# Kernel tuning notes

Hardware: AMD Instinct MI355X
Metric: run time of the kernel (lower is better)

## Reference

```python
import jax, jax.numpy as jnp
import numpy as np

B, L, D, H, FF, NS = 4, 1024, 1024, 16, 4096, 64
HD = D // H
EPS = 1e-5


def layer_norm(x, g, b):
    mu = jnp.mean(x, axis=-1, keepdims=True)
    var = jnp.mean(jnp.square(x - mu), axis=-1, keepdims=True)
    return (x - mu) * jax.lax.rsqrt(var + EPS) * g + b


def mha(xq, xkv, wqkv, bqkv, wo, bo, bias=None):
    # torch nn.MultiheadAttention with packed in_proj: rows [0:D]=Q, [D:2D]=K, [2D:3D]=V
    Bq, Lq, Dm = xq.shape
    q = (xq @ wqkv[:Dm].T + bqkv[:Dm]).reshape(Bq, Lq, H, HD).transpose(0, 2, 1, 3)
    k = (xkv @ wqkv[Dm:2 * Dm].T + bqkv[Dm:2 * Dm]).reshape(Bq, -1, H, HD).transpose(0, 2, 1, 3)
    v = (xkv @ wqkv[2 * Dm:].T + bqkv[2 * Dm:]).reshape(Bq, -1, H, HD).transpose(0, 2, 1, 3)
    scores = jnp.einsum('bhqd,bhkd->bhqk', q, k) / np.sqrt(HD).astype(np.float32)
    if bias is not None:
        scores = scores + bias.reshape(Bq, H, Lq, -1)
    attn = jax.nn.softmax(scores, axis=-1)
    out = jnp.einsum('bhqk,bhkd->bhqd', attn, v).transpose(0, 2, 1, 3).reshape(Bq, Lq, Dm)
    return out @ wo.T + bo


def setup_inputs() -> dict:
    key = jax.random.key(0)
    ks = jax.random.split(key, 16)
    w = lambda k, shape: jax.random.normal(k, shape, jnp.float32) * 0.02
    return {
        'x': jax.random.normal(ks[0], (B, L, D), jnp.float32),
        'alibi_bias': jax.random.normal(ks[1], (B * H, L, L), jnp.float32) * 0.1,
        'species_emb': jax.random.normal(ks[2], (B, NS, D), jnp.float32),
        'norm1_g': jnp.ones(D), 'norm1_b': jnp.zeros(D),
        'sa_wqkv': w(ks[3], (3 * D, D)), 'sa_bqkv': jnp.zeros(3 * D),
        'sa_wo': w(ks[4], (D, D)), 'sa_bo': jnp.zeros(D),
        'ca_nq_g': jnp.ones(D), 'ca_nq_b': jnp.zeros(D),
        'ca_nkv_g': jnp.ones(D), 'ca_nkv_b': jnp.zeros(D),
        'ca_wqkv': w(ks[5], (3 * D, D)), 'ca_bqkv': jnp.zeros(3 * D),
        'ca_wo': w(ks[6], (D, D)), 'ca_bo': jnp.zeros(D),
        'gate_param': jnp.float32(0.1),
        'ffn_g': jnp.ones(D), 'ffn_b': jnp.zeros(D),
        'ffn_w1': w(ks[7], (2 * FF, D)), 'ffn_b1': jnp.zeros(2 * FF),
        'ffn_w2': w(ks[8], (D, FF)), 'ffn_b2': jnp.zeros(D),
    }


def reference(x, alibi_bias, species_emb,
              norm1_g, norm1_b, sa_wqkv, sa_bqkv, sa_wo, sa_bo,
              ca_nq_g, ca_nq_b, ca_nkv_g, ca_nkv_b, ca_wqkv, ca_bqkv, ca_wo, ca_bo,
              gate_param, ffn_g, ffn_b, ffn_w1, ffn_b1, ffn_w2, ffn_b2):
    # 1) pre-norm self-attention with ALiBi additive bias
    h = layer_norm(x, norm1_g, norm1_b)
    h = mha(h, h, sa_wqkv, sa_bqkv, sa_wo, sa_bo, bias=alibi_bias)
    x = x + h  # dropout is identity in eval mode
    # 2) gated cross-attention with species embeddings
    q = layer_norm(x, ca_nq_g, ca_nq_b)
    kv = layer_norm(species_emb, ca_nkv_g, ca_nkv_b)
    cross = mha(q, kv, ca_wqkv, ca_bqkv, ca_wo, ca_bo)
    x = x + jax.nn.sigmoid(gate_param) * cross
    # 3) GEGLU feed-forward
    f = layer_norm(x, ffn_g, ffn_b) @ ffn_w1.T + ffn_b1
    val, gate = f[..., :FF], f[..., FF:]
    f = (val * jax.nn.gelu(gate, approximate=False)) @ ffn_w2.T + ffn_b2
    return x + f
```

## Files before the change

### kernel.cpp

```cpp
#include <hip/hip_runtime.h>
#include <hip/hip_bf16.h>
#include <cstdint>

#define DEVI __device__ __forceinline__

typedef __attribute__((ext_vector_type(8))) short  short8;
typedef __attribute__((ext_vector_type(8))) __bf16 bf16x8;
typedef __attribute__((ext_vector_type(4))) float  f32x4;

DEVI float bf2f(short s) {
    unsigned u = ((unsigned)(unsigned short)s) << 16;
    return __builtin_bit_cast(float, u);
}
DEVI short f2bf(float f) {
    unsigned u = __builtin_bit_cast(unsigned, f);
    u = u + 0x7FFF + ((u >> 16) & 1);
    return (short)(u >> 16);
}

#define GLDS(gp, lp) __builtin_amdgcn_global_load_lds( \
    (const __attribute__((address_space(1))) void*)(gp), \
    (__attribute__((address_space(3))) void*)(lp), 16, 0, 0)

__global__ __launch_bounds__(256) void cvt_bf16(const float* src, short* dst, long n) {
    const long i = ((long)blockIdx.x * 256 + threadIdx.x) * 8;
    const float4 a = *(const float4*)&src[i];
    const float4 b = *(const float4*)&src[i + 4];
    short8 o;
    o[0] = f2bf(a.x); o[1] = f2bf(a.y); o[2] = f2bf(a.z); o[3] = f2bf(a.w);
    o[4] = f2bf(b.x); o[5] = f2bf(b.y); o[6] = f2bf(b.z); o[7] = f2bf(b.w);
    *(short8*)&dst[i] = o;
}

struct CvtArgs {
    const float* src[6]; short* dst[6]; int blkStart[7];
};
__global__ __launch_bounds__(256) void cvt_all(CvtArgs c) {
    const int b = blockIdx.x;
    int s = 0;
    while (b >= c.blkStart[s + 1]) s++;
    const long i = ((long)(b - c.blkStart[s]) * 256 + threadIdx.x) * 8;
    const float4 a0 = *(const float4*)&c.src[s][i];
    const float4 a1 = *(const float4*)&c.src[s][i + 4];
    short8 o;
    o[0] = f2bf(a0.x); o[1] = f2bf(a0.y); o[2] = f2bf(a0.z); o[3] = f2bf(a0.w);
    o[4] = f2bf(a1.x); o[5] = f2bf(a1.y); o[6] = f2bf(a1.z); o[7] = f2bf(a1.w);
    *(short8*)&c.dst[s][i] = o;
}

struct GArgs {
    const short* A; long lda, sAb, sAh;
    const short* B; long ldb, sBb, sBh;
    short* C;       long ldc, sCb, sCh;
    const float* bias;
    const float* addm; long ldad, sDb, sDh;
    float* resid;
    float* outf;
    const float* gate;
    const float* addf;
    float scale;
    int K, nh;
};

template<int BM, int BN, int EPI>
__global__ __launch_bounds__(256) void gemm_bt(GArgs a) {
    constexpr int WM = BM / 2, WN = BN / 2, MI = WM / 16, NI = WN / 16;
    __shared__ __align__(16) short As[2][BM * 32];
    __shared__ __align__(16) short Bs[2][BN * 32];
    const int tid = threadIdx.x;
    const int wave = tid >> 6, lane = tid & 63;
    const int wm = (wave >> 1) * WM, wn = (wave & 1) * WN;
    const int q = lane >> 4, r = lane & 15;
    const int gx = gridDim.x, gy = gridDim.y;
    int flat = (int)(blockIdx.y * gx + blockIdx.x);
    { const int cp = (gx * gy) >> 3; flat = (flat & 7) * cp + (flat >> 3); }
    const int bx = flat % gx, by = flat / gx;
    const long bb = blockIdx.z / a.nh, hh = blockIdx.z % a.nh;
    const short* Ab = a.A + bb * a.sAb + hh * a.sAh + (long)by * BM * a.lda;
    const short* Bb = a.B + bb * a.sBb + hh * a.sBh + (long)bx * BN * a.ldb;
    const int trow = tid >> 2;
    const int tcol = (tid & 3) * 8;
    f32x4 acc[MI][NI] = {};
    const int nt = a.K >> 5;

    auto stage = [&](int buf, int k0) {
#pragma unroll
        for (int i = 0; i < BM / 64; i++)
            GLDS(Ab + (long)(i * 64 + trow) * a.lda + k0 + tcol,
                 &As[buf][(i * 64 + trow) * 32 + tcol]);
#pragma unroll
        for (int i = 0; i < BN / 64; i++)
            GLDS(Bb + (long)(i * 64 + trow) * a.ldb + k0 + tcol,
                 &Bs[buf][(i * 64 + trow) * 32 + tcol]);
    };

    stage(0, 0);
    asm volatile("s_waitcnt vmcnt(0)" ::: "memory");
    __builtin_amdgcn_s_barrier();

    int cur = 0;
    for (int t = 0; t < nt; ++t) {
        if (t + 1 < nt) stage(cur ^ 1, (t + 1) << 5);
        bf16x8 av[MI], bv[NI];
#pragma unroll
        for (int mi = 0; mi < MI; mi++)
            av[mi] = __builtin_bit_cast(bf16x8, *(const short8*)&As[cur][(wm + mi * 16 + r) * 32 + q * 8]);
#pragma unroll
        for (int ni = 0; ni < NI; ni++)
            bv[ni] = __builtin_bit_cast(bf16x8, *(const short8*)&Bs[cur][(wn + ni * 16 + r) * 32 + q * 8]);
#pragma unroll
        for (int mi = 0; mi < MI; mi++)
#pragma unroll
            for (int ni = 0; ni < NI; ni++)
                acc[mi][ni] = __builtin_amdgcn_mfma_f32_16x16x32_bf16(av[mi], bv[ni], acc[mi][ni], 0, 0, 0);
        asm volatile("s_waitcnt vmcnt(0) lgkmcnt(0)" ::: "memory");
        __builtin_amdgcn_s_barrier();
        cur ^= 1;
    }

    const long m0 = (long)by * BM + wm;
    const long n0 = (long)bx * BN + wn;
    if constexpr (EPI == 0) {
        short* scrbase = &As[0][0];
        short* scr = scrbase + wave * 16 * (WN + 2);
        short* Cbase = a.C + bb * a.sCb + hh * a.sCh;
        constexpr int LPR = WN / 8;
        constexpr int RPI = 64 / LPR;
        const int srow = lane / LPR, scol = (lane % LPR) * 8;
#pragma unroll
        for (int mi = 0; mi < MI; mi++) {
            asm volatile("s_waitcnt lgkmcnt(0)" ::: "memory");
#pragma unroll
            for (int ni = 0; ni < NI; ni++)
#pragma unroll
                for (int j = 0; j < 4; j++) {
                    float v = acc[mi][ni][j];
                    if (a.bias) v += a.bias[n0 + ni * 16 + r];
                    scr[(q * 4 + j) * (WN + 2) + ni * 16 + r] = f2bf(v);
                }
            asm volatile("s_waitcnt lgkmcnt(0)" ::: "memory");
#pragma unroll
            for (int it = 0; it < 16 / RPI; it++) {
                const int row = it * RPI + srow;
                const short8 vv = *(const short8*)&scr[row * (WN + 2) + scol];
                *(short8*)&Cbase[(m0 + mi * 16 + row) * a.ldc + n0 + scol] = vv;
            }
        }
        return;
    }
    float gs = a.scale;
    if (EPI == 2 && a.gate) gs *= 1.f / (1.f + __expf(-(*a.gate)));
#pragma unroll
    for (int mi = 0; mi < MI; mi++)
#pragma unroll
        for (int ni = 0; ni < NI; ni++)
#pragma unroll
            for (int j = 0; j < 4; j++) {
                const long m = m0 + mi * 16 + q * 4 + j;
                const long n = n0 + ni * 16 + r;
                float v = acc[mi][ni][j];
                if constexpr (EPI == 1) {
                    v *= a.scale;
                    if (a.addm) v += a.addm[bb * a.sDb + hh * a.sDh + m * a.ldad + n];
                    a.C[bb * a.sCb + hh * a.sCh + m * a.ldc + n] = f2bf(v);
                } else if constexpr (EPI == 2) {
                    if (a.bias) v += a.bias[n];
                    const long idx = m * a.ldc + n;
                    const float base = a.addf ? a.addf[idx] : a.resid[idx];
                    a.resid[idx] = base + gs * v;
                } else if constexpr (EPI == 3) {
                    if (a.bias) v += a.bias[n];
                    a.outf[m * a.ldc + n] = a.resid[m * a.ldc + n] + v;
                }
            }
}

struct GGArgs {
    const short* A; long lda;
    const short* Bv; const short* Bg; long ldb;
    short* C; long ldc;
    const float* b1;
    int K;
};
__global__ __launch_bounds__(256) void gemm_geglu(GGArgs a) {
    constexpr int BM = 128, BN = 64, WM = 64, WN = 32, MI = 4, NI = 2;
    __shared__ __align__(16) short As[2][BM * 32];
    __shared__ __align__(16) short Bs[2][BN * 32];
    __shared__ __align__(16) short Gs[2][BN * 32];
    const int tid = threadIdx.x;
    const int wave = tid >> 6, lane = tid & 63;
    const int wm = (wave >> 1) * WM, wn = (wave & 1) * WN;
    const int q = lane >> 4, r = lane & 15;
    const int gx = gridDim.x, gy = gridDim.y;
    int flat = (int)(blockIdx.y * gx + blockIdx.x);
    { const int cp = (gx * gy) >> 3; flat = (flat & 7) * cp + (flat >> 3); }
    const int bx = flat % gx, by = flat / gx;
    const short* Ab = a.A + (long)by * BM * a.lda;
    const short* Bb = a.Bv + (long)bx * BN * a.ldb;
    const short* Gb = a.Bg + (long)bx * BN * a.ldb;
    const int trow = tid >> 2, tcol = (tid & 3) * 8;
    f32x4 accv[MI][NI] = {}, accg[MI][NI] = {};
    const int nt = a.K >> 5;

    auto stage = [&](int buf, int k0) {
#pragma unroll
        for (int i = 0; i < 2; i++)
            GLDS(Ab + (long)(i * 64 + trow) * a.lda + k0 + tcol,
                 &As[buf][(i * 64 + trow) * 32 + tcol]);
        GLDS(Bb + (long)trow * a.ldb + k0 + tcol, &Bs[buf][trow * 32 + tcol]);
        GLDS(Gb + (long)trow * a.ldb + k0 + tcol, &Gs[buf][trow * 32 + tcol]);
    };

    stage(0, 0);
    asm volatile("s_waitcnt vmcnt(0)" ::: "memory");
    __builtin_amdgcn_s_barrier();

    int cur = 0;
    for (int t = 0; t < nt; ++t) {
        if (t + 1 < nt) stage(cur ^ 1, (t + 1) << 5);
        bf16x8 av[MI], bv[NI], gv[NI];
#pragma unroll
        for (int mi = 0; mi < MI; mi++)
            av[mi] = __builtin_bit_cast(bf16x8, *(const short8*)&As[cur][(wm + mi * 16 + r) * 32 + q * 8]);
#pragma unroll
        for (int ni = 0; ni < NI; ni++) {
            bv[ni] = __builtin_bit_cast(bf16x8, *(const short8*)&Bs[cur][(wn + ni * 16 + r) * 32 + q * 8]);
            gv[ni] = __builtin_bit_cast(bf16x8, *(const short8*)&Gs[cur][(wn + ni * 16 + r) * 32 + q * 8]);
        }
#pragma unroll
        for (int mi = 0; mi < MI; mi++)
#pragma unroll
            for (int ni = 0; ni < NI; ni++) {
                accv[mi][ni] = __builtin_amdgcn_mfma_f32_16x16x32_bf16(av[mi], bv[ni], accv[mi][ni], 0, 0, 0);
                accg[mi][ni] = __builtin_amdgcn_mfma_f32_16x16x32_bf16(av[mi], gv[ni], accg[mi][ni], 0, 0, 0);
            }
        asm volatile("s_waitcnt vmcnt(0) lgkmcnt(0)" ::: "memory");
        __builtin_amdgcn_s_barrier();
        cur ^= 1;
    }

    const long m0 = (long)by * BM + wm;
    const long n0 = (long)bx * BN + wn;
    short* scr = &As[0][0] + wave * 16 * (WN + 2);
    const int srow = lane >> 2, scol = (lane & 3) * 8;
#pragma unroll
    for (int mi = 0; mi < MI; mi++) {
        asm volatile("s_waitcnt lgkmcnt(0)" ::: "memory");
#pragma unroll
        for (int ni = 0; ni < NI; ni++)
#pragma unroll
            for (int j = 0; j < 4; j++) {
                const long n = n0 + ni * 16 + r;
                const float v = accv[mi][ni][j] + a.b1[n];
                const float g = accg[mi][ni][j] + a.b1[4096 + n];
                const float ge = 0.5f * g * (1.f + erff(g * 0.7071067811865476f));
                scr[(q * 4 + j) * (WN + 2) + ni * 16 + r] = f2bf(v * ge);
            }
        asm volatile("s_waitcnt lgkmcnt(0)" ::: "memory");
        const short8 vv = *(const short8*)&scr[srow * (WN + 2) + scol];
        *(short8*)&a.C[(m0 + mi * 16 + srow) * a.ldc + n0 + scol] = vv;
    }
}

__global__ __launch_bounds__(256) void flash_sa(const short* qkv, const short* vt,
                                                const float* alibi, short* Obuf) {
    __shared__ __align__(16) short Ps[64 * 64];
    __shared__ __align__(16) short Ks[2][64 * 64], Vs[2][64 * 64];
    const int tid = threadIdx.x;
    const int wave = tid >> 6, lane = tid & 63, q = lane >> 4, r = lane & 15;
    int flat = (int)(blockIdx.y * 16 + blockIdx.x);
    flat = (flat & 7) * 128 + (flat >> 3);
    const int qt = flat & 15, bh = flat >> 4, b = bh >> 4, h = bh & 15;
    const long qrow0 = (long)b * 1024 + qt * 64;
    const int rw = tid >> 3, sp = tid & 7;

    auto stage_kv = [&](int buf, int kt) {
#pragma unroll
        for (int i = 0; i < 2; i++) {
            const int row = i * 32 + rw;
            const int c8 = (sp ^ (row & 7)) * 8;
            GLDS(qkv + ((long)b * 1024 + kt * 64 + row) * 3072 + 1024 + h * 64 + c8,
                 &Ks[buf][row * 64 + sp * 8]);
            GLDS(vt + ((long)bh * 64 + row) * 1024 + kt * 64 + c8,
                 &Vs[buf][row * 64 + sp * 8]);
        }
    };

#pragma unroll
    for (int i = 0; i < 2; i++) {
        const int row = i * 32 + rw;
        const int c8 = (sp ^ (row & 7)) * 8;
        GLDS(qkv + (qrow0 + row) * 3072 + h * 64 + c8, &Ps[row * 64 + sp * 8]);
    }
    stage_kv(0, 0);
    asm volatile("s_waitcnt vmcnt(0)" ::: "memory");
    __builtin_amdgcn_s_barrier();

    const int arow = wave * 16 + r;
    bf16x8 qv[2];
#pragma unroll
    for (int kk = 0; kk < 2; kk++)
        qv[kk] = __builtin_bit_cast(bf16x8,
            *(const short8*)&Ps[arow * 64 + (((kk * 4 + q) ^ (arow & 7)) * 8)]);

    f32x4 o[4] = {};
    float m_run[4], l_run[4];
#pragma unroll
    for (int j = 0; j < 4; j++) { m_run[j] = -1e30f; l_run[j] = 0.f; }

    int cur = 0;
    for (int kt = 0; kt < 16; kt++) {
        float al[4][4];
        const float* ab = alibi + (long)bh * 1048576 + (long)(qt * 64 + wave * 16) * 1024 + kt * 64;
#pragma unroll
        for (int ni = 0; ni < 4; ni++)
#pragma unroll
            for (int j = 0; j < 4; j++)
                al[ni][j] = ab[(q * 4 + j) * 1024 + ni * 16 + r];
        if (kt < 15) stage_kv(cur ^ 1, kt + 1);

        f32x4 sacc[4] = {};
        __builtin_amdgcn_s_setprio(1);
#pragma unroll
        for (int kk = 0; kk < 2; kk++) {
#pragma unroll
            for (int ni = 0; ni < 4; ni++) {
                const int brow = ni * 16 + r;
                const bf16x8 bv = __builtin_bit_cast(bf16x8,
                    *(const short8*)&Ks[cur][brow * 64 + (((kk * 4 + q) ^ (brow & 7)) * 8)]);
                sacc[ni] = __builtin_amdgcn_mfma_f32_16x16x32_bf16(qv[kk], bv, sacc[ni], 0, 0, 0);
            }
        }
        __builtin_amdgcn_s_setprio(0);
        float s[4][4];
#pragma unroll
        for (int ni = 0; ni < 4; ni++)
#pragma unroll
            for (int j = 0; j < 4; j++)
                s[ni][j] = sacc[ni][j] * 0.125f + al[ni][j];

        float p[4][4];
#pragma unroll
        for (int j = 0; j < 4; j++) {
            float mx = fmaxf(fmaxf(s[0][j], s[1][j]), fmaxf(s[2][j], s[3][j]));
#pragma unroll
            for (int off = 8; off; off >>= 1) mx = fmaxf(mx, __shfl_xor(mx, off));
            const float newm = fmaxf(m_run[j], mx);
            const float sc = __expf(m_run[j] - newm);
            m_run[j] = newm;
            float rs = 0.f;
#pragma unroll
            for (int ni = 0; ni < 4; ni++) { p[ni][j] = __expf(s[ni][j] - newm); rs += p[ni][j]; }
#pragma unroll
            for (int off = 8; off; off >>= 1) rs += __shfl_xor(rs, off);
            l_run[j] = l_run[j] * sc + rs;
#pragma unroll
            for (int nd = 0; nd < 4; nd++) o[nd][j] *= sc;
        }

#pragma unroll
        for (int ni = 0; ni < 4; ni++)
#pragma unroll
            for (int j = 0; j < 4; j++) {
                const int row = wave * 16 + q * 4 + j;
                const int col = ni * 16 + r;
                const int scol = (((col >> 3) ^ (row & 7)) << 3) | (col & 7);
                Ps[row * 64 + scol] = f2bf(p[ni][j]);
            }
        asm volatile("s_waitcnt lgkmcnt(0)" ::: "memory");

        const int prow = wave * 16 + r;
        __builtin_amdgcn_s_setprio(1);
#pragma unroll
        for (int kk = 0; kk < 2; kk++) {
            const bf16x8 pa = __builtin_bit_cast(bf16x8,
                *(const short8*)&Ps[prow * 64 + (((kk * 4 + q) ^ (prow & 7)) * 8)]);
#pragma unroll
            for (int nd = 0; nd < 4; nd++) {
                const int vrow = nd * 16 + r;
                const bf16x8 vv = __builtin_bit_cast(bf16x8,
                    *(const short8*)&Vs[cur][vrow * 64 + (((kk * 4 + q) ^ (vrow & 7)) * 8)]);
                o[nd] = __builtin_amdgcn_mfma_f32_16x16x32_bf16(pa, vv, o[nd], 0, 0, 0);
            }
        }
        __builtin_amdgcn_s_setprio(0);
        asm volatile("s_waitcnt vmcnt(0) lgkmcnt(0)" ::: "memory");
        __builtin_amdgcn_s_barrier();
        cur ^= 1;
    }

    short* scr = &Ps[wave * 1024];
#pragma unroll
    for (int j = 0; j < 4; j++) {
        const float li = 1.f / l_run[j];
#pragma unroll
        for (int nd = 0; nd < 4; nd++)
            scr[(q * 4 + j) * 64 + nd * 16 + r] = f2bf(o[nd][j] * li);
    }
    asm volatile("s_waitcnt lgkmcnt(0)" ::: "memory");
    const int srow = lane >> 3, scol = (lane & 7) * 8;
#pragma unroll
    for (int it = 0; it < 2; it++) {
        const int row = it * 8 + srow;
        const short8 vv = *(const short8*)&scr[row * 64 + scol];
        *(short8*)&Obuf[(qrow0 + wave * 16 + row) * 1024 + h * 64 + scol] = vv;
    }
}

__global__ __launch_bounds__(256) void flash_ca(const short* q2, const short* kv2,
                                                const short* vt, short* Obuf) {
    __shared__ __align__(16) short Qs[64 * 64], Ks[64 * 64], Vs[64 * 64], Ps[64 * 64];
    const int tid = threadIdx.x;
    const int wave = tid >> 6, lane = tid & 63, q = lane >> 4, r = lane & 15;
    int flat = (int)(blockIdx.y * 16 + blockIdx.x);
    flat = (flat & 7) * 128 + (flat >> 3);
    const int qt = flat & 15, bh = flat >> 4, b = bh >> 4, h = bh & 15;
    const long qrow0 = (long)b * 1024 + qt * 64;
    const int rw = tid >> 3, sp = tid & 7;

#pragma unroll
    for (int i = 0; i < 2; i++) {
        const int row = i * 32 + rw;
        const int c8 = (sp ^ (row & 7)) * 8;
        GLDS(q2 + (qrow0 + row) * 1024 + h * 64 + c8, &Qs[row * 64 + sp * 8]);
        GLDS(kv2 + ((long)b * 64 + row) * 2048 + h * 64 + c8, &Ks[row * 64 + sp * 8]);
        GLDS(vt + ((long)bh * 64 + row) * 64 + c8, &Vs[row * 64 + sp * 8]);
    }
    asm volatile("s_waitcnt vmcnt(0)" ::: "memory");
    __syncthreads();

    f32x4 sacc[4] = {};
    const int arow = wave * 16 + r;
    __builtin_amdgcn_s_setprio(1);
#pragma unroll
    for (int kk = 0; kk < 2; kk++) {
        const bf16x8 av = __builtin_bit_cast(bf16x8,
            *(const short8*)&Qs[arow * 64 + (((kk * 4 + q) ^ (arow & 7)) * 8)]);
#pragma unroll
        for (int ni = 0; ni < 4; ni++) {
            const int brow = ni * 16 + r;
            const bf16x8 bv = __builtin_bit_cast(bf16x8,
                *(const short8*)&Ks[brow * 64 + (((kk * 4 + q) ^ (brow & 7)) * 8)]);
            sacc[ni] = __builtin_amdgcn_mfma_f32_16x16x32_bf16(av, bv, sacc[ni], 0, 0, 0);
        }
    }
    __builtin_amdgcn_s_setprio(0);
    float p[4][4], linv[4];
#pragma unroll
    for (int j = 0; j < 4; j++) {
        float s0 = sacc[0][j] * 0.125f, s1 = sacc[1][j] * 0.125f;
        float s2 = sacc[2][j] * 0.125f, s3 = sacc[3][j] * 0.125f;
        float mx = fmaxf(fmaxf(s0, s1), fmaxf(s2, s3));
#pragma unroll
        for (int off = 8; off; off >>= 1) mx = fmaxf(mx, __shfl_xor(mx, off));
        p[0][j] = __expf(s0 - mx); p[1][j] = __expf(s1 - mx);
        p[2][j] = __expf(s2 - mx); p[3][j] = __expf(s3 - mx);
        float rs = p[0][j] + p[1][j] + p[2][j] + p[3][j];
#pragma unroll
        for (int off = 8; off; off >>= 1) rs += __shfl_xor(rs, off);
        linv[j] = 1.f / rs;
    }
#pragma unroll
    for (int ni = 0; ni < 4; ni++)
#pragma unroll
        for (int j = 0; j < 4; j++) {
            const int row = wave * 16 + q * 4 + j;
            const int col = ni * 16 + r;
            const int scol = (((col >> 3) ^ (row & 7)) << 3) | (col & 7);
            Ps[row * 64 + scol] = f2bf(p[ni][j]);
        }
    asm volatile("s_waitcnt lgkmcnt(0)" ::: "memory");

    f32x4 o[4] = {};
    const int prow = wave * 16 + r;
    __builtin_amdgcn_s_setprio(1);
#pragma unroll
    for (int kk = 0; kk < 2; kk++) {
        const bf16x8 pa = __builtin_bit_cast(bf16x8,
            *(const short8*)&Ps[prow * 64 + (((kk * 4 + q) ^ (prow & 7)) * 8)]);
#pragma unroll
        for (int nd = 0; nd < 4; nd++) {
            const int vrow = nd * 16 + r;
            const bf16x8 vv = __builtin_bit_cast(bf16x8,
                *(const short8*)&Vs[vrow * 64 + (((kk * 4 + q) ^ (vrow & 7)) * 8)]);
            o[nd] = __builtin_amdgcn_mfma_f32_16x16x32_bf16(pa, vv, o[nd], 0, 0, 0);
        }
    }
    __builtin_amdgcn_s_setprio(0);

    short* scr = &Ps[wave * 1024];
#pragma unroll
    for (int j = 0; j < 4; j++)
#pragma unroll
        for (int nd = 0; nd < 4; nd++)
            scr[(q * 4 + j) * 64 + nd * 16 + r] = f2bf(o[nd][j] * linv[j]);
    asm volatile("s_waitcnt lgkmcnt(0)" ::: "memory");
    const int srow = lane >> 3, scol = (lane & 7) * 8;
#pragma unroll
    for (int it = 0; it < 2; it++) {
        const int row = it * 8 + srow;
        const short8 vv = *(const short8*)&scr[row * 64 + scol];
        *(short8*)&Obuf[(qrow0 + wave * 16 + row) * 1024 + h * 64 + scol] = vv;
    }
}

__global__ __launch_bounds__(256) void ln_rows(const float* X, const float* gw,
                                               const float* bw, short* Y) {
    const long row = blockIdx.x;
    const float* x = X + row * 1024;
    const int t = threadIdx.x;
    float v[4], s1 = 0.f, s2 = 0.f;
#pragma unroll
    for (int i = 0; i < 4; i++) {
        v[i] = x[t + i * 256];
        s1 += v[i]; s2 += v[i] * v[i];
    }
#pragma unroll
    for (int o = 32; o; o >>= 1) { s1 += __shfl_xor(s1, o); s2 += __shfl_xor(s2, o); }
    __shared__ float sm[8];
    if ((t & 63) == 0) { sm[t >> 6] = s1; sm[4 + (t >> 6)] = s2; }
    __syncthreads();
    s1 = sm[0] + sm[1] + sm[2] + sm[3];
    s2 = sm[4] + sm[5] + sm[6] + sm[7];
    const float mu = s1 * (1.f / 1024.f);
    const float var = s2 * (1.f / 1024.f) - mu * mu;
    const float rr = rsqrtf(var + 1e-5f);
#pragma unroll
    for (int i = 0; i < 4; i++) {
        const int c = t + i * 256;
        Y[row * 1024 + c] = f2bf((v[i] - mu) * rr * gw[c] + bw[c]);
    }
}

__global__ __launch_bounds__(256) void softmax1024(short* S) {
    const long row = blockIdx.x;
    short* p = S + row * 1024;
    const int t = threadIdx.x;
    float v[4];
#pragma unroll
    for (int i = 0; i < 4; i++) v[i] = bf2f(p[t + i * 256]);
    float m = fmaxf(fmaxf(v[0], v[1]), fmaxf(v[2], v[3]));
#pragma unroll
    for (int o = 32; o; o >>= 1) m = fmaxf(m, __shfl_xor(m, o));
    __shared__ float sm[4];
    if ((t & 63) == 0) sm[t >> 6] = m;
    __syncthreads();
    m = fmaxf(fmaxf(sm[0], sm[1]), fmaxf(sm[2], sm[3]));
    float e[4], s = 0.f;
#pragma unroll
    for (int i = 0; i < 4; i++) { e[i] = __expf(v[i] - m); s += e[i]; }
#pragma unroll
    for (int o = 32; o; o >>= 1) s += __shfl_xor(s, o);
    __syncthreads();
    if ((t & 63) == 0) sm[t >> 6] = s;
    __syncthreads();
    s = sm[0] + sm[1] + sm[2] + sm[3];
    const float inv = 1.f / s;
#pragma unroll
    for (int i = 0; i < 4; i++) p[t + i * 256] = f2bf(e[i] * inv);
}

__global__ __launch_bounds__(256) void softmax64(short* S) {
    const long row = (long)blockIdx.x * 4 + (threadIdx.x >> 6);
    const int lane = threadIdx.x & 63;
    short* p = S + row * 64;
    float v = bf2f(p[lane]);
    float m = v;
#pragma unroll
    for (int o = 32; o; o >>= 1) m = fmaxf(m, __shfl_xor(m, o));
    float e = __expf(v - m), s = e;
#pragma unroll
    for (int o = 32; o; o >>= 1) s += __shfl_xor(s, o);
    p[lane] = f2bf(e / s);
}

__global__ __launch_bounds__(256) void transpose_v_sa(const short* qkv, short* vt) {
    __shared__ short tbuf[64][68];
    const int j0 = blockIdx.x * 64, h = blockIdx.y, b = blockIdx.z;
    const int tid = threadIdx.x;
#pragma unroll
    for (int i = 0; i < 16; i++) {
        const int idx = i * 256 + tid, jj = idx >> 6, hd = idx & 63;
        tbuf[jj][hd] = qkv[(long)(b * 1024 + j0 + jj) * 3072 + 2048 + h * 64 + hd];
    }
    __syncthreads();
    const long bh = b * 16 + h;
#pragma unroll
    for (int i = 0; i < 16; i++) {
        const int idx = i * 256 + tid, hd = idx >> 6, jj = idx & 63;
        vt[(bh * 64 + hd) * 1024 + j0 + jj] = tbuf[jj][hd];
    }
}

__global__ __launch_bounds__(256) void transpose_v_ca(const short* kv2, short* vt2) {
    __shared__ short tbuf[64][68];
    const int bh = blockIdx.x, b = bh >> 4, h = bh & 15;
    const int tid = threadIdx.x;
#pragma unroll
    for (int i = 0; i < 16; i++) {
        const int idx = i * 256 + tid, jj = idx >> 6, hd = idx & 63;
        tbuf[jj][hd] = kv2[(long)(b * 64 + jj) * 2048 + 1024 + h * 64 + hd];
    }
    __syncthreads();
#pragma unroll
    for (int i = 0; i < 16; i++) {
        const int idx = i * 256 + tid, hd = idx >> 6, jj = idx & 63;
        vt2[((long)bh * 64 + hd) * 64 + jj] = tbuf[jj][hd];
    }
}

__global__ __launch_bounds__(256) void geglu_inplace(short* f1) {
    const long i = (long)blockIdx.x * 256 + threadIdx.x;
    const long m = i >> 9, j8 = (i & 511) * 8;
    const short8 av = *(const short8*)&f1[m * 8192 + j8];
    const short8 gv = *(const short8*)&f1[m * 8192 + 4096 + j8];
    short8 o;
#pragma unroll
    for (int jj = 0; jj < 8; jj++) {
        const float xv = bf2f(av[jj]), gg = bf2f(gv[jj]);
        const float ge = 0.5f * gg * (1.f + erff(gg * 0.7071067811865476f));
        o[jj] = f2bf(xv * ge);
    }
    *(short8*)&f1[m * 8192 + j8] = o;
}

extern "C" void kernel_launch(void* const* d_in, const int* in_sizes, int n_in,
                              void* d_out, int out_size, void* d_ws, size_t ws_size,
                              hipStream_t stream) {
    const float* x        = (const float*)d_in[0];
    const float* alibi    = (const float*)d_in[1];
    const float* species  = (const float*)d_in[2];
    const float* n1g      = (const float*)d_in[3];
    const float* n1b      = (const float*)d_in[4];
    const float* sa_wqkv  = (const float*)d_in[5];
    const float* sa_bqkv  = (const float*)d_in[6];
    const float* sa_wo    = (const float*)d_in[7];
    const float* sa_bo    = (const float*)d_in[8];
    const float* ca_nq_g  = (const float*)d_in[9];
    const float* ca_nq_b  = (const float*)d_in[10];
    const float* ca_nkv_g = (const float*)d_in[11];
    const float* ca_nkv_b = (const float*)d_in[12];
    const float* ca_wqkv  = (const float*)d_in[13];
    const float* ca_bqkv  = (const float*)d_in[14];
    const float* ca_wo    = (const float*)d_in[15];
    const float* ca_bo    = (const float*)d_in[16];
    const float* gate     = (const float*)d_in[17];
    const float* ffn_g    = (const float*)d_in[18];
    const float* ffn_b    = (const float*)d_in[19];
    const float* ffn_w1   = (const float*)d_in[20];
    const float* ffn_b1   = (const float*)d_in[21];
    const float* ffn_w2   = (const float*)d_in[22];
    const float* ffn_b2   = (const float*)d_in[23];
    float* out = (float*)d_out;

    const dim3 blk(256);
    char* ws = (char*)d_ws;

    if (ws_size >= (304ull << 20)) {
        float* resid  = (float*)(ws);
        short* lnbuf  = (short*)(ws + (16l << 20));
        short* Obuf   = (short*)(ws + (24l << 20));
        short* vt     = (short*)(ws + (32l << 20));
        short* qkv    = (short*)(ws + (40l << 20));
        short* w_saq  = (short*)(ws + (64l << 20));
        short* w_sawo = (short*)(ws + (70l << 20));
        short* w_caq  = (short*)(ws + (72l << 20));
        short* w_cawo = (short*)(ws + (78l << 20));
        short* w_f1   = (short*)(ws + (80l << 20));
        short* w_f2   = (short*)(ws + (96l << 20));
        short* kv2    = (short*)(ws + (104l << 20));
        short* g1     = (short*)(ws + (240l << 20));

        {
            CvtArgs c{};
            c.src[0] = sa_wqkv; c.dst[0] = w_saq;
            c.src[1] = sa_wo;   c.dst[1] = w_sawo;
            c.src[2] = ca_wqkv; c.dst[2] = w_caq;
            c.src[3] = ca_wo;   c.dst[3] = w_cawo;
            c.src[4] = ffn_w1;  c.dst[4] = w_f1;
            c.src[5] = ffn_w2;  c.dst[5] = w_f2;
            const int nb[6] = {1536, 512, 1536, 512, 4096, 2048};
            int acc = 0;
            for (int i = 0; i < 6; i++) { c.blkStart[i] = acc; acc += nb[i]; }
            c.blkStart[6] = acc;
            cvt_all<<<acc, blk, 0, stream>>>(c);
        }

        ln_rows<<<4096, blk, 0, stream>>>(x, n1g, n1b, lnbuf);

        {
            GArgs a{}; a.A = lnbuf; a.lda = 1024; a.B = w_saq; a.ldb = 1024;
            a.C = qkv; a.ldc = 3072; a.bias = sa_bqkv; a.K = 1024; a.nh = 1; a.scale = 1.f;
            gemm_bt<128, 128, 0><<<dim3(24, 32, 1), blk, 0, stream>>>(a);
        }
        transpose_v_sa<<<dim3(16, 16, 4), blk, 0, stream>>>(qkv, vt);

        flash_sa<<<dim3(16, 64), blk, 0, stream>>>(qkv, vt, alibi, Obuf);

        {
            GArgs a{}; a.A = Obuf; a.lda = 1024; a.B = w_sawo; a.ldb = 1024;
            a.ldc = 1024; a.bias = sa_bo; a.resid = resid; a.addf = x;
            a.scale = 1.f; a.K = 1024; a.nh = 1;
            gemm_bt<128, 64, 2><<<dim3(16, 32, 1), blk, 0, stream>>>(a);
        }

        ln_rows<<<4096, blk, 0, stream>>>(resid, ca_nq_g, ca_nq_b, lnbuf);
        {
            GArgs a{}; a.A = lnbuf; a.lda = 1024; a.B = w_caq; a.ldb = 1024;
            a.C = qkv; a.ldc = 1024; a.bias = ca_bqkv; a.K = 1024; a.nh = 1; a.scale = 1.f;
            gemm_bt<128, 64, 0><<<dim3(16, 32, 1), blk, 0, stream>>>(a);
        }
        ln_rows<<<256, blk, 0, stream>>>(species, ca_nkv_g, ca_nkv_b, lnbuf);
        {
            GArgs a{}; a.A = lnbuf; a.lda = 1024; a.B = w_caq + 1024 * 1024; a.ldb = 1024;
            a.C = kv2; a.ldc = 2048; a.bias = ca_bqkv + 1024; a.K = 1024; a.nh = 1; a.scale = 1.f;
            gemm_bt<128, 128, 0><<<dim3(16, 2, 1), blk, 0, stream>>>(a);
        }
        transpose_v_ca<<<64, blk, 0, stream>>>(kv2, vt);

        flash_ca<<<dim3(16, 64), blk, 0, stream>>>(qkv, kv2, vt, Obuf);

        {
            GArgs a{}; a.A = Obuf; a.lda = 1024; a.B = w_cawo; a.ldb = 1024;
            a.ldc = 1024; a.bias = ca_bo; a.resid = resid; a.gate = gate;
            a.scale = 1.f; a.K = 1024; a.nh = 1;
            gemm_bt<128, 64, 2><<<dim3(16, 32, 1), blk, 0, stream>>>(a);
        }

        ln_rows<<<4096, blk, 0, stream>>>(resid, ffn_g, ffn_b, lnbuf);
        {
            GGArgs a{}; a.A = lnbuf; a.lda = 1024;
            a.Bv = w_f1; a.Bg = w_f1 + (long)4096 * 1024; a.ldb = 1024;
            a.C = g1; a.ldc = 4096; a.b1 = ffn_b1; a.K = 1024;
            gemm_geglu<<<dim3(64, 32, 1), blk, 0, stream>>>(a);
        }
        {
            GArgs a{}; a.A = g1; a.lda = 4096; a.B = w_f2; a.ldb = 4096;
            a.ldc = 1024; a.bias = ffn_b2; a.resid = resid; a.outf = out;
            a.scale = 1.f; a.K = 4096; a.nh = 1;
            gemm_bt<128, 64, 3><<<dim3(16, 32, 1), blk, 0, stream>>>(a);
        }
        return;
    }

    float* resid  = (float*)(ws);
    short* lnbuf  = (short*)(ws + (16l << 20));
    short* Obuf   = (short*)(ws + (24l << 20));
    short* vt     = (short*)(ws + (32l << 20));
    short* qkv    = (short*)(ws + (40l << 20));
    short* Sbuf   = (short*)(ws + (64l << 20));
    short* f1     = Sbuf;
    short* kv2    = qkv + 4194304;
    short* w_sawo = (short*)(ws + (80l << 20));
    short* w_caq  = (short*)(ws + (82l << 20));
    short* w_cawo = (short*)(ws + (88l << 20));
    short* w_saq  = (short*)(ws + (90l << 20));
    short* w_f1   = qkv;
    short* w_f2   = (short*)(ws + (56l << 20));

    cvt_bf16<<<1536, blk, 0, stream>>>(sa_wqkv, w_saq, 3145728);
    cvt_bf16<<<512,  blk, 0, stream>>>(sa_wo,   w_sawo, 1048576);
    cvt_bf16<<<1536, blk, 0, stream>>>(ca_wqkv, w_caq, 3145728);
    cvt_bf16<<<512,  blk, 0, stream>>>(ca_wo,   w_cawo, 1048576);

    hipMemcpyAsync(resid, x, (size_t)4194304 * 4, hipMemcpyDeviceToDevice, stream);
    ln_rows<<<4096, blk, 0, stream>>>(x, n1g, n1b, lnbuf);

    {
        GArgs a{}; a.A = lnbuf; a.lda = 1024; a.B = w_saq; a.ldb = 1024;
        a.C = qkv; a.ldc = 3072; a.bias = sa_bqkv; a.K = 1024; a.nh = 1; a.scale = 1.f;
        gemm_bt<128, 128, 0><<<dim3(24, 32, 1), blk, 0, stream>>>(a);
    }
    transpose_v_sa<<<dim3(16, 16, 4), blk, 0, stream>>>(qkv, vt);

    for (int c = 0; c < 8; c++) {
        const int b = c >> 1, hc = c & 1;
        const long boff = (long)b * 1024 * 3072;
        {
            GArgs a{}; a.A = qkv + boff + hc * 512; a.lda = 3072; a.sAh = 64;
            a.B = qkv + boff + 1024 + hc * 512; a.ldb = 3072; a.sBh = 64;
            a.C = Sbuf; a.ldc = 1024; a.sCh = 1048576;
            a.addm = alibi + ((long)(b * 16 + hc * 8)) * 1048576; a.ldad = 1024; a.sDh = 1048576;
            a.scale = 0.125f; a.K = 64; a.nh = 8;
            gemm_bt<128, 128, 1><<<dim3(8, 8, 8), blk, 0, stream>>>(a);
        }
        softmax1024<<<8192, blk, 0, stream>>>(Sbuf);
        {
            GArgs a{}; a.A = Sbuf; a.lda = 1024; a.sAh = 1048576;
            a.B = vt + (long)b * 1048576 + (long)hc * 8 * 65536; a.ldb = 1024; a.sBh = 65536;
            a.C = Obuf + (long)b * 1048576 + hc * 512; a.ldc = 1024; a.sCh = 64;
            a.K = 1024; a.nh = 8; a.scale = 1.f;
            gemm_bt<64, 64, 0><<<dim3(1, 16, 8), blk, 0, stream>>>(a);
        }
    }
    {
        GArgs a{}; a.A = Obuf; a.lda = 1024; a.B = w_sawo; a.ldb = 1024;
        a.ldc = 1024; a.bias = sa_bo; a.resid = resid; a.scale = 1.f; a.K = 1024; a.nh = 1;
        gemm_bt<128, 128, 2><<<dim3(8, 32, 1), blk, 0, stream>>>(a);
    }

    ln_rows<<<4096, blk, 0, stream>>>(resid, ca_nq_g, ca_nq_b, lnbuf);
    {
        GArgs a{}; a.A = lnbuf; a.lda = 1024; a.B = w_caq; a.ldb = 1024;
        a.C = qkv; a.ldc = 1024; a.bias = ca_bqkv; a.K = 1024; a.nh = 1; a.scale = 1.f;
        gemm_bt<128, 128, 0><<<dim3(8, 32, 1), blk, 0, stream>>>(a);
    }
    ln_rows<<<256, blk, 0, stream>>>(species, ca_nkv_g, ca_nkv_b, lnbuf);
    {
        GArgs a{}; a.A = lnbuf; a.lda = 1024; a.B = w_caq + 1024 * 1024; a.ldb = 1024;
        a.C = kv2; a.ldc = 2048; a.bias = ca_bqkv + 1024; a.K = 1024; a.nh = 1; a.scale = 1.f;
        gemm_bt<128, 128, 0><<<dim3(16, 2, 1), blk, 0, stream>>>(a);
    }
    transpose_v_ca<<<64, blk, 0, stream>>>(kv2, vt);
    {
        GArgs a{}; a.A = qkv; a.lda = 1024; a.sAb = 1048576; a.sAh = 64;
        a.B = kv2; a.ldb = 2048; a.sBb = 131072; a.sBh = 64;
        a.C = Sbuf; a.ldc = 64; a.sCb = 1048576; a.sCh = 65536;
        a.scale = 0.125f; a.K = 64; a.nh = 16;
        gemm_bt<64, 64, 1><<<dim3(1, 16, 64), blk, 0, stream>>>(a);
    }
    cvt_bf16<<<4096, blk, 0, stream>>>(ffn_w1, w_f1, 8388608);
    cvt_bf16<<<2048, blk, 0, stream>>>(ffn_w2, w_f2, 4194304);

    softmax64<<<16384, blk, 0, stream>>>(Sbuf);
    {
        GArgs a{}; a.A = Sbuf; a.lda = 64; a.sAb = 1048576; a.sAh = 65536;
        a.B = vt; a.ldb = 64; a.sBb = 65536; a.sBh = 4096;
        a.C = Obuf; a.ldc = 1024; a.sCb = 1048576; a.sCh = 64;
        a.K = 64; a.nh = 16; a.scale = 1.f;
        gemm_bt<64, 64, 0><<<dim3(1, 16, 64), blk, 0, stream>>>(a);
    }
    {
        GArgs a{}; a.A = Obuf; a.lda = 1024; a.B = w_cawo; a.ldb = 1024;
        a.ldc = 1024; a.bias = ca_bo; a.resid = resid; a.gate = gate;
        a.scale = 1.f; a.K = 1024; a.nh = 1;
        gemm_bt<128, 128, 2><<<dim3(8, 32, 1), blk, 0, stream>>>(a);
    }

    ln_rows<<<4096, blk, 0, stream>>>(resid, ffn_g, ffn_b, lnbuf);
    for (int rc = 0; rc < 2; rc++) {
        const long ro = (long)rc * 2048;
        {
            GArgs a{}; a.A = lnbuf + ro * 1024; a.lda = 1024; a.B = w_f1; a.ldb = 1024;
            a.C = f1; a.ldc = 8192; a.bias = ffn_b1; a.K = 1024; a.nh = 1; a.scale = 1.f;
            gemm_bt<128, 128, 0><<<dim3(64, 16, 1), blk, 0, stream>>>(a);
        }
        geglu_inplace<<<4096, blk, 0, stream>>>(f1);
        {
            GArgs a{}; a.A = f1; a.lda = 8192; a.B = w_f2; a.ldb = 4096;
            a.ldc = 1024; a.bias = ffn_b2; a.resid = resid + ro * 1024; a.outf = out + ro * 1024;
            a.scale = 1.f; a.K = 4096; a.nh = 1;
            gemm_bt<128, 64, 3><<<dim3(8, 16, 1), blk, 0, stream>>>(a);
        }
    }
}
```

Measured before the change: 898.6 us.

## Fuse V transpose into QKV GEMM epilogue and widen GEGLU tile

The QKV projection GEMM epilogue now writes the V columns straight into the transposed per-head layout through a swizzled LDS staging buffer, which removes the separate transpose_v_sa launch and its extra read and write of V. The GEGLU GEMM tile is widened from 64 to 128 columns, so each block reuses its A tile across twice as many outputs and the grid is halved. In exchange the larger tile uses more LDS and registers per block and may lower occupancy. The V columns are also no longer written in normal layout to qkv, which is safe only if nothing else reads them.

```diff
diff --git a/kernel.cpp b/kernel.cpp
--- a/kernel.cpp
+++ b/kernel.cpp
@@ -58,6 +58,7 @@
     float* outf;
     const float* gate;
     const float* addf;
+    short* vtr;
     float scale;
     int K, nh;
 };
@@ -121,6 +122,44 @@
     const long m0 = (long)by * BM + wm;
     const long n0 = (long)bx * BN + wn;
     if constexpr (EPI == 0) {
+        if constexpr (BM == 128 && BN == 128) {
+            const long nblk = (long)bx * BN;
+            if (a.vtr && nblk >= 2048) {
+                short* T = &As[0][0];
+                const long mblk = (long)by * BM;
+                const int mloc = (int)(mblk & 1023);
+                const int h0 = (int)((nblk - 2048) >> 6);
+                const int hsel = wn >> 6;
+#pragma unroll
+                for (int hh2 = 0; hh2 < 2; hh2++) {
+                    __syncthreads();
+                    if (hsel == hh2) {
+#pragma unroll
+                        for (int mi = 0; mi < MI; mi++)
+#pragma unroll
+                            for (int ni = 0; ni < NI; ni++)
+#pragma unroll
+                                for (int j = 0; j < 4; j++) {
+                                    float v = acc[mi][ni][j] + a.bias[n0 + ni * 16 + r];
+                                    const int hd = ni * 16 + r;
+                                    const int jl = wm + mi * 16 + q * 4 + j;
+                                    const int cj = jl >> 3, jj2 = jl & 7;
+                                    T[hd * 128 + ((cj ^ (hd & 7)) << 3) + jj2] = f2bf(v);
+                                }
+                    }
+                    __syncthreads();
+                    const long bh = (mblk >> 10) * 16 + h0 + hh2;
+#pragma unroll
+                    for (int it = 0; it < 4; it++) {
+                        const int c = it * 256 + tid;
+                        const int hd = c >> 4, ch = c & 15;
+                        const short8 vv = *(const short8*)&T[hd * 128 + ((ch ^ (hd & 7)) << 3)];
+                        *(short8*)&a.vtr[(bh * 64 + hd) * 1024 + mloc + ch * 8] = vv;
+                    }
+                }
+                return;
+            }
+        }
         short* scrbase = &As[0][0];
         short* scr = scrbase + wave * 16 * (WN + 2);
         short* Cbase = a.C + bb * a.sCb + hh * a.sCh;
@@ -183,7 +222,7 @@
     int K;
 };
 __global__ __launch_bounds__(256) void gemm_geglu(GGArgs a) {
-    constexpr int BM = 128, BN = 64, WM = 64, WN = 32, MI = 4, NI = 2;
+    constexpr int BM = 128, BN = 128, WM = 64, WN = 64, MI = 4, NI = 4;
     __shared__ __align__(16) short As[2][BM * 32];
     __shared__ __align__(16) short Bs[2][BN * 32];
     __shared__ __align__(16) short Gs[2][BN * 32];
@@ -204,11 +243,14 @@
 
     auto stage = [&](int buf, int k0) {
 #pragma unroll
-        for (int i = 0; i < 2; i++)
+        for (int i = 0; i < 2; i++) {
             GLDS(Ab + (long)(i * 64 + trow) * a.lda + k0 + tcol,
                  &As[buf][(i * 64 + trow) * 32 + tcol]);
-        GLDS(Bb + (long)trow * a.ldb + k0 + tcol, &Bs[buf][trow * 32 + tcol]);
-        GLDS(Gb + (long)trow * a.ldb + k0 + tcol, &Gs[buf][trow * 32 + tcol]);
+            GLDS(Bb + (long)(i * 64 + trow) * a.ldb + k0 + tcol,
+                 &Bs[buf][(i * 64 + trow) * 32 + tcol]);
+            GLDS(Gb + (long)(i * 64 + trow) * a.ldb + k0 + tcol,
+                 &Gs[buf][(i * 64 + trow) * 32 + tcol]);
+        }
     };
 
     stage(0, 0);
@@ -242,7 +284,8 @@
     const long m0 = (long)by * BM + wm;
     const long n0 = (long)bx * BN + wn;
     short* scr = &As[0][0] + wave * 16 * (WN + 2);
-    const int srow = lane >> 2, scol = (lane & 3) * 8;
+    constexpr int LPR = WN / 8, RPI = 64 / LPR;
+    const int srow = lane / LPR, scol = (lane % LPR) * 8;
 #pragma unroll
     for (int mi = 0; mi < MI; mi++) {
         asm volatile("s_waitcnt lgkmcnt(0)" ::: "memory");
@@ -257,8 +300,12 @@
                 scr[(q * 4 + j) * (WN + 2) + ni * 16 + r] = f2bf(v * ge);
             }
         asm volatile("s_waitcnt lgkmcnt(0)" ::: "memory");
-        const short8 vv = *(const short8*)&scr[srow * (WN + 2) + scol];
-        *(short8*)&a.C[(m0 + mi * 16 + srow) * a.ldc + n0 + scol] = vv;
+#pragma unroll
+        for (int it = 0; it < 16 / RPI; it++) {
+            const int row = it * RPI + srow;
+            const short8 vv = *(const short8*)&scr[row * (WN + 2) + scol];
+            *(short8*)&a.C[(m0 + mi * 16 + row) * a.ldc + n0 + scol] = vv;
+        }
     }
 }
 
@@ -690,10 +737,10 @@
 
         {
             GArgs a{}; a.A = lnbuf; a.lda = 1024; a.B = w_saq; a.ldb = 1024;
-            a.C = qkv; a.ldc = 3072; a.bias = sa_bqkv; a.K = 1024; a.nh = 1; a.scale = 1.f;
+            a.C = qkv; a.ldc = 3072; a.bias = sa_bqkv; a.vtr = vt;
+            a.K = 1024; a.nh = 1; a.scale = 1.f;
             gemm_bt<128, 128, 0><<<dim3(24, 32, 1), blk, 0, stream>>>(a);
         }
-        transpose_v_sa<<<dim3(16, 16, 4), blk, 0, stream>>>(qkv, vt);
 
         flash_sa<<<dim3(16, 64), blk, 0, stream>>>(qkv, vt, alibi, Obuf);
 
@@ -732,7 +779,7 @@
             GGArgs a{}; a.A = lnbuf; a.lda = 1024;
             a.Bv = w_f1; a.Bg = w_f1 + (long)4096 * 1024; a.ldb = 1024;
             a.C = g1; a.ldc = 4096; a.b1 = ffn_b1; a.K = 1024;
-            gemm_geglu<<<dim3(64, 32, 1), blk, 0, stream>>>(a);
+            gemm_geglu<<<dim3(32, 32, 1), blk, 0, stream>>>(a);
         }
         {
             GArgs a{}; a.A = g1; a.lda = 4096; a.B = w_f2; a.ldb = 4096;
```

New measurement: 984.0 us. 1.1x slower.
